# Optimization experiments

Measured on AMD Instinct MI355X. Metric: run time of the kernel, lower is better.

## Reference

```python
import jax, jax.numpy as jnp
import numpy as np
import math

B, S, D = 1, 4096, 512
H, KVH, DH = 8, 4, 64
DH2 = DH // 2
M = int(math.isqrt(S))           # product-key grid side, S == M*M
K = 8                            # top_k
ROPE_BASE = 10000.0


def rope_cos_sin(seq_len, dh, base):
    inv_freq = 1.0 / (base ** (jnp.arange(0, dh, 2, dtype=jnp.float32) / dh))
    t = jnp.arange(seq_len, dtype=jnp.float32)
    freqs = jnp.outer(t, inv_freq)                      # (S, dh/2)
    emb = jnp.concatenate([freqs, freqs], axis=-1)      # (S, dh)
    return jnp.cos(emb), jnp.sin(emb)


def apply_rope(x, cos, sin):
    # x: (B, H, S, dh); half-split rotation (llama-style)
    dh2 = x.shape[-1] // 2
    rot = jnp.concatenate([-x[..., dh2:], x[..., :dh2]], axis=-1)
    return x * cos + rot * sin


def setup_inputs() -> dict:
    key = jax.random.key(0)
    ks = jax.random.split(key, 5)
    s = 0.02
    x = jax.random.normal(ks[0], (B, S, D), dtype=jnp.float32)
    Wq = jax.random.normal(ks[1], (H * DH, D), dtype=jnp.float32) * s
    Wk = jax.random.normal(ks[2], (KVH * DH, D), dtype=jnp.float32) * s
    Wv = jax.random.normal(ks[3], (KVH * DH, D), dtype=jnp.float32) * s
    Wo = jax.random.normal(ks[4], (D, H * DH), dtype=jnp.float32) * s
    return {"x": x, "Wq": Wq, "Wk": Wk, "Wv": Wv, "Wo": Wo}


def reference(x, Wq, Wk, Wv, Wo):
    b, s, d = x.shape
    cos, sin = rope_cos_sin(s, DH, ROPE_BASE)
    q = (x @ Wq.T).reshape(b, s, H, DH).transpose(0, 2, 1, 3)      # (B,H,S,DH)
    k = (x @ Wk.T).reshape(b, s, KVH, DH).transpose(0, 2, 1, 3)    # (B,KVH,S,DH)
    v = (x @ Wv.T).reshape(b, s, KVH, DH).transpose(0, 2, 1, 3)
    q = apply_rope(q, cos, sin)
    k = apply_rope(k, cos, sin)
    rep = H // KVH                                                 # GQA repeat_kv
    k = jnp.repeat(k, rep, axis=1)                                 # (B,H,S,DH)
    v = jnp.repeat(v, rep, axis=1)

    # factorized product keys: sum over grid rows / cols
    kg = k.reshape(b, H, M, M, DH)
    k1 = kg[..., :DH2].sum(axis=-2)                                # (B,H,M,DH2)
    k2 = kg[..., DH2:].sum(axis=-3)                                # (B,H,M,DH2)
    q1, q2 = q[..., :DH2], q[..., DH2:]

    def topk_sel(qh, kh):  # qh: (S,DH2), kh: (M,DH2)
        scores = qh @ kh.T                                         # (S,M)
        _, idx = jax.lax.top_k(scores, K)                          # (S,K)
        return kh[idx], idx                                        # (S,K,DH2), (S,K)

    sel2 = jax.vmap(jax.vmap(topk_sel))
    k1v, i1 = sel2(q1, k1)                                         # (B,H,S,K,DH2)
    k2v, i2 = sel2(q2, k2)

    # cross-product candidates: (B,H,S,K,K,DH) -> (B,H,S,K*K,DH)
    c1 = jnp.broadcast_to(k1v[:, :, :, :, None, :], (b, H, s, K, K, DH2))
    c2 = jnp.broadcast_to(k2v[:, :, :, None, :, :], (b, H, s, K, K, DH2))
    cand = jnp.concatenate([c1, c2], axis=-1).reshape(b, H, s, K * K, DH)

    scores_final = jnp.einsum('bhsd,bhscd->bhsc', q, cand)         # (B,H,S,K*K)
    _, sel = jax.lax.top_k(scores_final, K)                        # (B,H,S,K)
    final_k = jnp.take_along_axis(cand, sel[..., None], axis=3)    # (B,H,S,K,DH)

    row = jnp.take_along_axis(i1, sel // K, axis=3)
    col = jnp.take_along_axis(i2, sel % K, axis=3)
    v_idx = row * M + col                                          # (B,H,S,K)
    final_v = jax.vmap(jax.vmap(lambda vb, ib: vb[ib]))(v, v_idx)  # (B,H,S,K,DH)

    attn = jax.nn.softmax(
        jnp.einsum('bhsd,bhskd->bhsk', q, final_k) / math.sqrt(DH), axis=-1)
    o = jnp.einsum('bhsk,bhskd->bhsd', attn, final_v)              # (B,H,S,DH)
    o = o.transpose(0, 2, 1, 3).reshape(b, s, H * DH)
    return o @ Wo.T
```

## Files before the change

### kernel.cpp

```cpp
#include <hip/hip_runtime.h>
#include <math.h>


static constexpr size_t OFF_P1   = 0;
static constexpr size_t OFF_P2   = 4194304;
static constexpr size_t OFF_KB   = 8388608;
static constexpr size_t OFF_V    = 9437184;
static constexpr size_t OFF_COS  = 10485760;
static constexpr size_t OFF_SIN  = 10616832;
static constexpr size_t OFF_K1   = 10747904;
static constexpr size_t OFF_K2   = 10756096;
static constexpr size_t OFF_O    = 10764288;
static constexpr size_t OFF_PACK = 12861440;

#define LDB 132
#define TILE_F (16 * LDB)

__device__ __forceinline__ float rdlane_f(float v, int lane) {
  return __int_as_float(__builtin_amdgcn_readlane(__float_as_int(v), lane));
}

__global__ __launch_bounds__(256) void freq_table_kernel(float* __restrict__ cosT,
    float* __restrict__ sinT) {
  int idx = blockIdx.x * 256 + threadIdx.x;
  int s = idx >> 5;
  int dp = idx & 31;
  double e = (double)dp * (1.0 / 32.0);
  float pf = (float)pow(10000.0, e);
  float invf = 1.0f / pf;
  float argf = __fmul_rn((float)s, invf);
  cosT[idx] = (float)cos((double)argf);
  sinT[idx] = (float)sin((double)argf);
}

__global__ __launch_bounds__(512) void gemm128_qkv(const float* __restrict__ A,
    const float* __restrict__ Wq, const float* __restrict__ Wk,
    const float* __restrict__ Wv, float* __restrict__ C1,
    float* __restrict__ C2) {
  __shared__ float As[2 * TILE_F];
  __shared__ float Bs[2 * TILE_F];
  const int tid = threadIdx.x;
  const int z = blockIdx.z;
  const int k0 = z ? 384 : 0;
  const int k1 = z ? 512 : 384;
  float* __restrict__ C = z ? C2 : C1;
  const int bm = blockIdx.y, bn = blockIdx.x;
  const int lrow = tid >> 2;
  const int lko = (tid & 3) << 2;
  const int ty = tid >> 4;
  const int tx = tid & 15;
  const float* Bbase = (bn < 4) ? (Wq + ((size_t)bn * 128) * 512)
                     : (bn < 6) ? (Wk + ((size_t)(bn - 4) * 128) * 512)
                                : (Wv + ((size_t)(bn - 6) * 128) * 512);
  const float* Ap = A + (size_t)(bm * 128 + lrow) * 512 + lko;
  const float* Bp = Bbase + (size_t)lrow * 512 + lko;
  float acc[4][8] = {{0.f}};
  float4 a0 = *(const float4*)(Ap + k0);
  float4 b0 = *(const float4*)(Bp + k0);
  int p = 0;
  for (int kt = k0; kt < k1; kt += 16) {
    float* Asp = As + p * TILE_F;
    float* Bsp = Bs + p * TILE_F;
    Asp[(lko + 0) * LDB + lrow] = a0.x;
    Asp[(lko + 1) * LDB + lrow] = a0.y;
    Asp[(lko + 2) * LDB + lrow] = a0.z;
    Asp[(lko + 3) * LDB + lrow] = a0.w;
    Bsp[(lko + 0) * LDB + lrow] = b0.x;
    Bsp[(lko + 1) * LDB + lrow] = b0.y;
    Bsp[(lko + 2) * LDB + lrow] = b0.z;
    Bsp[(lko + 3) * LDB + lrow] = b0.w;
    __syncthreads();
    if (kt + 16 < k1) {
      a0 = *(const float4*)(Ap + kt + 16);
      b0 = *(const float4*)(Bp + kt + 16);
    }
    #pragma unroll
    for (int k = 0; k < 16; ++k) {
      float4 av = *(const float4*)(&Asp[k * LDB + (ty << 2)]);
      float4 bl = *(const float4*)(&Bsp[k * LDB + (tx << 2)]);
      float4 bh = *(const float4*)(&Bsp[k * LDB + 64 + (tx << 2)]);
      float af[4] = {av.x, av.y, av.z, av.w};
      float bf[8] = {bl.x, bl.y, bl.z, bl.w, bh.x, bh.y, bh.z, bh.w};
      #pragma unroll
      for (int i2 = 0; i2 < 4; ++i2)
        #pragma unroll
        for (int j2 = 0; j2 < 8; ++j2)
          acc[i2][j2] = fmaf(af[i2], bf[j2], acc[i2][j2]);
    }
    p ^= 1;
  }
  #pragma unroll
  for (int i2 = 0; i2 < 4; ++i2) {
    int row = bm * 128 + (ty << 2) + i2;
    float* Cp = C + (size_t)row * 1024 + bn * 128;
    *(float4*)(Cp + (tx << 2))      = make_float4(acc[i2][0], acc[i2][1], acc[i2][2], acc[i2][3]);
    *(float4*)(Cp + 64 + (tx << 2)) = make_float4(acc[i2][4], acc[i2][5], acc[i2][6], acc[i2][7]);
  }
}

__global__ __launch_bounds__(512) void gemm128_out(const float* __restrict__ A,
    const float* __restrict__ B, float* __restrict__ Cbase, int N) {
  __shared__ float As[2 * TILE_F];
  __shared__ float Bs[2 * TILE_F];
  const int tid = threadIdx.x;
  const int z = blockIdx.z;
  const int k0 = z << 7;
  const int k1 = k0 + 128;
  float* __restrict__ C = Cbase + (size_t)z * ((size_t)4096 * N);
  const int bm = blockIdx.y, bn = blockIdx.x;
  const int lrow = tid >> 2;
  const int lko = (tid & 3) << 2;
  const int ty = tid >> 4;
  const int tx = tid & 15;
  const float* Ap = A + (size_t)(bm * 128 + lrow) * 512 + lko;
  const float* Bp = B + (size_t)(bn * 128 + lrow) * 512 + lko;
  float acc[4][8] = {{0.f}};
  float4 a0 = *(const float4*)(Ap + k0);
  float4 b0 = *(const float4*)(Bp + k0);
  int p = 0;
  for (int kt = k0; kt < k1; kt += 16) {
    float* Asp = As + p * TILE_F;
    float* Bsp = Bs + p * TILE_F;
    Asp[(lko + 0) * LDB + lrow] = a0.x;
    Asp[(lko + 1) * LDB + lrow] = a0.y;
    Asp[(lko + 2) * LDB + lrow] = a0.z;
    Asp[(lko + 3) * LDB + lrow] = a0.w;
    Bsp[(lko + 0) * LDB + lrow] = b0.x;
    Bsp[(lko + 1) * LDB + lrow] = b0.y;
    Bsp[(lko + 2) * LDB + lrow] = b0.z;
    Bsp[(lko + 3) * LDB + lrow] = b0.w;
    __syncthreads();
    if (kt + 16 < k1) {
      a0 = *(const float4*)(Ap + kt + 16);
      b0 = *(const float4*)(Bp + kt + 16);
    }
    #pragma unroll
    for (int k = 0; k < 16; ++k) {
      float4 av = *(const float4*)(&Asp[k * LDB + (ty << 2)]);
      float4 bl = *(const float4*)(&Bsp[k * LDB + (tx << 2)]);
      float4 bh = *(const float4*)(&Bsp[k * LDB + 64 + (tx << 2)]);
      float af[4] = {av.x, av.y, av.z, av.w};
      float bf[8] = {bl.x, bl.y, bl.z, bl.w, bh.x, bh.y, bh.z, bh.w};
      #pragma unroll
      for (int i2 = 0; i2 < 4; ++i2)
        #pragma unroll
        for (int j2 = 0; j2 < 8; ++j2)
          acc[i2][j2] = fmaf(af[i2], bf[j2], acc[i2][j2]);
    }
    p ^= 1;
  }
  #pragma unroll
  for (int i2 = 0; i2 < 4; ++i2) {
    int row = bm * 128 + (ty << 2) + i2;
    float* Cp = C + (size_t)row * N + bn * 128;
    *(float4*)(Cp + (tx << 2))      = make_float4(acc[i2][0], acc[i2][1], acc[i2][2], acc[i2][3]);
    *(float4*)(Cp + 64 + (tx << 2)) = make_float4(acc[i2][4], acc[i2][5], acc[i2][6], acc[i2][7]);
  }
}

__global__ __launch_bounds__(256) void combine4_kernel(const float* __restrict__ o0,
    const float* __restrict__ o1, const float* __restrict__ o2,
    const float* __restrict__ o3, float* __restrict__ out) {
  int i = blockIdx.x * 256 + threadIdx.x;
  out[i] = __fadd_rn(__fadd_rn(__fadd_rn(o0[i], o1[i]), o2[i]), o3[i]);
}

__global__ __launch_bounds__(256) void kv_rope_kernel(const float* __restrict__ p1,
    const float* __restrict__ p2, const float* __restrict__ cosT,
    const float* __restrict__ sinT, float* __restrict__ kb,
    float* __restrict__ vb) {
  int id = blockIdx.x * 256 + threadIdx.x;
  int s = id >> 9;
  int n = 512 + (id & 511);
  int idx = (s << 10) + n;
  float val = __fadd_rn(p1[idx], p2[idx]);
  int d = n & 63;
  if (n < 768) {
    int pidx = idx ^ 32;
    float pv = __fadd_rn(p1[pidx], p2[pidx]);
    float cs = cosT[(s << 5) + (d & 31)];
    float sn = sinT[(s << 5) + (d & 31)];
    float rot = (d < 32) ? -pv : pv;
    float out = __fadd_rn(__fmul_rn(val, cs), __fmul_rn(rot, sn));
    int kvh = (n - 512) >> 6;
    kb[((size_t)(kvh * 4096 + s) << 6) + d] = out;
  } else {
    int kvh = (n - 768) >> 6;
    vb[((size_t)(kvh * 4096 + s) << 6) + d] = val;
  }
}

__global__ __launch_bounds__(256) void k12_np_kernel(const float* __restrict__ kb,
    float* __restrict__ k1t, float* __restrict__ k2t) {
  int id = blockIdx.x * 256 + threadIdx.x;
  int which = id >> 13;
  int rem = id & 8191;
  int kvh = rem >> 11;
  int rem2 = rem & 2047;
  int i = rem2 >> 5;
  int d = rem2 & 31;
  const float* base = kb + ((size_t)(kvh * 4096) << 6);
  if (which == 0) {
    float acc = base[((size_t)(i * 64) << 6) + d];
    for (int c = 1; c < 64; ++c)
      acc = __fadd_rn(acc, base[((size_t)(i * 64 + c) << 6) + d]);
    k1t[(kvh * 64 + i) * 32 + d] = acc;
  } else {
    float acc = base[((size_t)i << 6) + d + 32];
    for (int r = 1; r < 64; ++r)
      acc = __fadd_rn(acc, base[((size_t)(r * 64 + i) << 6) + d + 32]);
    k2t[(kvh * 64 + i) * 32 + d] = acc;
  }
}

__global__ __launch_bounds__(256) void stage1_sel_kernel(
    const float* __restrict__ p1, const float* __restrict__ p2,
    const float* __restrict__ cosT, const float* __restrict__ sinT,
    const float* __restrict__ k1t, const float* __restrict__ k2t,
    unsigned long long* __restrict__ packs) {
  __shared__ float smem[8704];
  float* qs = smem;
  float* kd = smem + 4352;
  const int t = threadIdx.x;
  const int h = blockIdx.y;
  const int s0 = blockIdx.x * 64;
  const int kvh = h >> 1;
  #pragma unroll
  for (int i = 0; i < 16; ++i) {
    int j = t + i * 256;
    int ss = j >> 6, d = j & 63;
    int s = s0 + ss;
    int idx = (s << 10) + (h << 6) + d;
    float val = __fadd_rn(p1[idx], p2[idx]);
    float pv  = __fadd_rn(p1[idx ^ 32], p2[idx ^ 32]);
    float cs = cosT[(s << 5) + (d & 31)];
    float sn = sinT[(s << 5) + (d & 31)];
    float rot = (d < 32) ? -pv : pv;
    qs[d * 68 + ss] = __fadd_rn(__fmul_rn(val, cs), __fmul_rn(rot, sn));
  }
  #pragma unroll
  for (int i = 0; i < 8; ++i) {
    int j = t + i * 256;
    int r = j >> 5, d = j & 31;
    kd[d * 132 + r]      = k1t[(kvh * 64 + r) * 32 + d];
    kd[d * 132 + 64 + r] = k2t[(kvh * 64 + r) * 32 + d];
  }
  __syncthreads();
  const int ty = t >> 4;
  const int tx = t & 15;
  float acc1[4][4] = {{0.f}};
  float acc2[4][4] = {{0.f}};
  #pragma unroll
  for (int dp = 0; dp < 32; ++dp) {
    float4 kv1 = *(const float4*)&kd[dp * 132 + (ty << 2)];
    float4 kv2 = *(const float4*)&kd[dp * 132 + 64 + (ty << 2)];
    float4 q1 = *(const float4*)&qs[dp * 68 + (tx << 2)];
    float4 q2 = *(const float4*)&qs[(32 + dp) * 68 + (tx << 2)];
    float k1f[4] = {kv1.x, kv1.y, kv1.z, kv1.w};
    float k2f[4] = {kv2.x, kv2.y, kv2.z, kv2.w};
    float q1f[4] = {q1.x, q1.y, q1.z, q1.w};
    float q2f[4] = {q2.x, q2.y, q2.z, q2.w};
    #pragma unroll
    for (int i2 = 0; i2 < 4; ++i2)
      #pragma unroll
      for (int j2 = 0; j2 < 4; ++j2) {
        acc1[i2][j2] = fmaf(k1f[i2], q1f[j2], acc1[i2][j2]);
        acc2[i2][j2] = fmaf(k2f[i2], q2f[j2], acc2[i2][j2]);
      }
  }
  __syncthreads();
  float* sct = smem;
  #pragma unroll
  for (int i2 = 0; i2 < 4; ++i2) {
    int r = (ty << 2) + i2;
    *(float4*)&sct[(size_t)r * 68 + (tx << 2)] =
        make_float4(acc1[i2][0], acc1[i2][1], acc1[i2][2], acc1[i2][3]);
    *(float4*)&sct[(size_t)(64 + r) * 68 + (tx << 2)] =
        make_float4(acc2[i2][0], acc2[i2][1], acc2[i2][2], acc2[i2][3]);
  }
  __syncthreads();
  if (t < 128) {
    int set = t >> 6;
    int sq = t & 63;
    const float* p = sct + (size_t)(set << 6) * 68 + sq;
    float top[8];
    int idx[8];
    #pragma unroll
    for (int u = 0; u < 8; ++u) { top[u] = -INFINITY; idx[u] = 0; }
    #pragma unroll
    for (int r = 0; r < 64; ++r) {
      float v = p[(size_t)r * 68];
      int i = r;
      #pragma unroll
      for (int j = 0; j < 8; ++j) {
        bool gt = v > top[j];
        float tv = top[j]; int ti = idx[j];
        top[j] = gt ? v : tv;
        idx[j] = gt ? i : ti;
        v = gt ? tv : v;
        i = gt ? ti : i;
      }
    }
    unsigned long long pp = 0;
    #pragma unroll
    for (int u = 0; u < 8; ++u) pp |= (unsigned long long)idx[u] << (6 * u);
    packs[(((size_t)(h * 4096 + s0 + sq)) << 1) + set] = pp;
  }
}

__device__ __forceinline__ void bitonic64_val_desc(float& v, int lane) {
  #pragma unroll
  for (int k = 2; k <= 64; k <<= 1) {
    #pragma unroll
    for (int j = k >> 1; j >= 1; j >>= 1) {
      float ov = __shfl_xor(v, j, 64);
      bool up = ((lane & k) == 0) == ((lane & j) == 0);
      float mx = fmaxf(v, ov), mn = fminf(v, ov);
      v = up ? mx : mn;
    }
  }
}

__global__ __launch_bounds__(256) void attn_sel2_kernel(
    const ulonglong2* __restrict__ packs, const float* __restrict__ p1,
    const float* __restrict__ p2, const float* __restrict__ cosT,
    const float* __restrict__ sinT, const float* __restrict__ vb,
    const float* __restrict__ k1t, const float* __restrict__ k2t,
    float* __restrict__ ob) {
  const int lane = threadIdx.x & 63;
  const int w = blockIdx.x * 4 + (threadIdx.x >> 6);
  const int h = w >> 12;
  const int s = w & 4095;
  const int kvh = h >> 1;
  ulonglong2 pk = packs[w];
  const unsigned long long pack1 = pk.x, pack2 = pk.y;
  int qidx = (s << 10) + (h << 6) + lane;
  float vraw = __fadd_rn(p1[qidx], p2[qidx]);
  float pv = __shfl_xor(vraw, 32, 64);
  float cs = cosT[(s << 5) + (lane & 31)];
  float sn = sinT[(s << 5) + (lane & 31)];
  float rot = (lane < 32) ? -pv : pv;
  const float qv = __fadd_rn(__fmul_rn(vraw, cs), __fmul_rn(rot, sn));

  int r1 = (int)((pack1 >> (6 * (lane >> 3))) & 63);
  int r2 = (int)((pack2 >> (6 * (lane & 7))) & 63);
  const float* k1p = k1t + (size_t)(kvh * 64 + r1) * 32;
  const float* k2p = k2t + (size_t)(kvh * 64 + r2) * 32;
  float c = 0.f;
  #pragma unroll
  for (int dq = 0; dq < 32; dq += 4) {
    float4 kk = *(const float4*)(k1p + dq);
    c = __fadd_rn(c, __fmul_rn(rdlane_f(qv, dq + 0), kk.x));
    c = __fadd_rn(c, __fmul_rn(rdlane_f(qv, dq + 1), kk.y));
    c = __fadd_rn(c, __fmul_rn(rdlane_f(qv, dq + 2), kk.z));
    c = __fadd_rn(c, __fmul_rn(rdlane_f(qv, dq + 3), kk.w));
  }
  #pragma unroll
  for (int dq = 0; dq < 32; dq += 4) {
    float4 kk = *(const float4*)(k2p + dq);
    c = __fadd_rn(c, __fmul_rn(rdlane_f(qv, 32 + dq + 0), kk.x));
    c = __fadd_rn(c, __fmul_rn(rdlane_f(qv, 32 + dq + 1), kk.y));
    c = __fadd_rn(c, __fmul_rn(rdlane_f(qv, 32 + dq + 2), kk.z));
    c = __fadd_rn(c, __fmul_rn(rdlane_f(qv, 32 + dq + 3), kk.w));
  }
  const float scand = c;
  float v3 = c;
  bitonic64_val_desc(v3, lane);
  float cvs[8]; int ccs[8];
  unsigned long long used = 0;
  #pragma unroll
  for (int t = 0; t < 8; ++t) {
    float tv = rdlane_f(v3, t);
    unsigned long long m = __ballot(scand == tv) & ~used;
    int ix = __ffsll((long long)m) - 1;
    used |= 1ull << ix;
    cvs[t] = tv;
    ccs[t] = ix;
  }
  float y[8];
  #pragma unroll
  for (int t = 0; t < 8; ++t) y[t] = cvs[t] * 0.125f;
  float mx = y[0];
  #pragma unroll
  for (int t = 1; t < 8; ++t) if (y[t] > mx) mx = y[t];
  float e[8];
  #pragma unroll
  for (int t = 0; t < 8; ++t) e[t] = __expf(__fsub_rn(y[t], mx));
  float wsum = __fadd_rn(__fadd_rn(__fadd_rn(e[0], e[1]), __fadd_rn(e[2], e[3])),
                         __fadd_rn(__fadd_rn(e[4], e[5]), __fadd_rn(e[6], e[7])));
  const float* vbh = vb + ((size_t)kvh << 18);
  float o = 0.f;
  #pragma unroll
  for (int t = 0; t < 8; ++t) {
    float att = __fdiv_rn(e[t], wsum);
    int row = (int)((pack1 >> (6 * (ccs[t] >> 3))) & 63);
    int col = (int)((pack2 >> (6 * (ccs[t] & 7))) & 63);
    o = __fadd_rn(o, __fmul_rn(att, vbh[((size_t)(row * 64 + col) << 6) + lane]));
  }
  ob[(size_t)s * 512 + (h << 6) + lane] = o;
}

extern "C" void kernel_launch(void* const* d_in, const int* in_sizes, int n_in,
                              void* d_out, int out_size, void* d_ws, size_t ws_size,
                              hipStream_t stream) {
  const float* x  = (const float*)d_in[0];
  const float* Wq = (const float*)d_in[1];
  const float* Wk = (const float*)d_in[2];
  const float* Wv = (const float*)d_in[3];
  const float* Wo = (const float*)d_in[4];
  float* ws = (float*)d_ws;
  float* p1   = ws + OFF_P1;
  float* p2   = ws + OFF_P2;
  float* kb   = ws + OFF_KB;
  float* vb   = ws + OFF_V;
  float* cosT = ws + OFF_COS;
  float* sinT = ws + OFF_SIN;
  float* k1t  = ws + OFF_K1;
  float* k2t  = ws + OFF_K2;
  float* ob   = ws + OFF_O;
  unsigned long long* packs = (unsigned long long*)(ws + OFF_PACK);
  float* op = ws + OFF_P1;

  freq_table_kernel<<<512, 256, 0, stream>>>(cosT, sinT);
  gemm128_qkv<<<dim3(8, 32, 2), 512, 0, stream>>>(x, Wq, Wk, Wv, p1, p2);
  kv_rope_kernel<<<8192, 256, 0, stream>>>(p1, p2, cosT, sinT, kb, vb);
  k12_np_kernel<<<64, 256, 0, stream>>>(kb, k1t, k2t);
  stage1_sel_kernel<<<dim3(64, 8), 256, 0, stream>>>(p1, p2, cosT, sinT, k1t, k2t, packs);
  attn_sel2_kernel<<<8192, 256, 0, stream>>>((const ulonglong2*)packs, p1, p2,
                                             cosT, sinT, vb, k1t, k2t, ob);
  gemm128_out<<<dim3(4, 32, 4), 512, 0, stream>>>(ob, Wo, op, 512);
  combine4_kernel<<<8192, 256, 0, stream>>>(op, op + 2097152, op + 4194304,
                                            op + 6291456, (float*)d_out);
}
```

Before: 242.4 us.

## Restructure projection GEMMs to stage only weights in LDS and stream activations

Both the QKV and output projection GEMMs are rewritten so that only a 16x256 weight tile goes through shared memory. Each wave now reads its 8 activation rows directly from global memory as wave-uniform float4 loads, prefetched one k-step ahead. Tiles change from 128x128 to 64x256 and the grid is resized to match. This halves LDS footprint and removes the A-tile stores and barriers. In exchange, activations are re-read from global or cache by every wave, and there is less per-thread register reuse (8x4 outputs per thread).

```diff
diff --git a/kernel.cpp b/kernel.cpp
--- a/kernel.cpp
+++ b/kernel.cpp
@@ -13,8 +13,10 @@
 static constexpr size_t OFF_O    = 10764288;
 static constexpr size_t OFF_PACK = 12861440;
 
-#define LDB 132
-#define TILE_F (16 * LDB)
+#define LDW 256
+#define WTILE (16 * LDW)
+
+#define COMP(v, j) ((j) == 0 ? (v).x : (j) == 1 ? (v).y : (j) == 2 ? (v).z : (v).w)
 
 __device__ __forceinline__ float rdlane_f(float v, int lane) {
   return __int_as_float(__builtin_amdgcn_readlane(__float_as_int(v), lane));
@@ -33,128 +35,155 @@
   sinT[idx] = (float)sin((double)argf);
 }
 
-__global__ __launch_bounds__(512) void gemm128_qkv(const float* __restrict__ A,
+__global__ __launch_bounds__(512, 4) void gemm_qkv_sA(const float* __restrict__ A,
     const float* __restrict__ Wq, const float* __restrict__ Wk,
     const float* __restrict__ Wv, float* __restrict__ C1,
     float* __restrict__ C2) {
-  __shared__ float As[2 * TILE_F];
-  __shared__ float Bs[2 * TILE_F];
+  __shared__ float Ws[2 * WTILE];
   const int tid = threadIdx.x;
   const int z = blockIdx.z;
   const int k0 = z ? 384 : 0;
-  const int k1 = z ? 512 : 384;
+  const int kend = z ? 512 : 384;
   float* __restrict__ C = z ? C2 : C1;
-  const int bm = blockIdx.y, bn = blockIdx.x;
-  const int lrow = tid >> 2;
-  const int lko = (tid & 3) << 2;
-  const int ty = tid >> 4;
-  const int tx = tid & 15;
-  const float* Bbase = (bn < 4) ? (Wq + ((size_t)bn * 128) * 512)
-                     : (bn < 6) ? (Wk + ((size_t)(bn - 4) * 128) * 512)
-                                : (Wv + ((size_t)(bn - 6) * 128) * 512);
-  const float* Ap = A + (size_t)(bm * 128 + lrow) * 512 + lko;
-  const float* Bp = Bbase + (size_t)lrow * 512 + lko;
-  float acc[4][8] = {{0.f}};
-  float4 a0 = *(const float4*)(Ap + k0);
-  float4 b0 = *(const float4*)(Bp + k0);
+  const int bn = blockIdx.x;
+  const int bm = blockIdx.y;
+  const int sn = tid & 255;
+  const int sk = (tid >> 8) << 3;
+  const float* Wbase = (bn < 2) ? (Wq + ((size_t)(bn * 256)) * 512)
+                     : (bn == 2) ? Wk : Wv;
+  const float* Wp = Wbase + (size_t)sn * 512 + sk;
+  const int wid = __builtin_amdgcn_readfirstlane(tid >> 6);
+  const float* Ab = A + (size_t)(bm * 64 + wid * 8) * 512;
+  const int lane = tid & 63;
+  float acc[8][4] = {{0.f}};
+  float4 g0 = *(const float4*)(Wp + k0);
+  float4 g1 = *(const float4*)(Wp + k0 + 4);
   int p = 0;
-  for (int kt = k0; kt < k1; kt += 16) {
-    float* Asp = As + p * TILE_F;
-    float* Bsp = Bs + p * TILE_F;
-    Asp[(lko + 0) * LDB + lrow] = a0.x;
-    Asp[(lko + 1) * LDB + lrow] = a0.y;
-    Asp[(lko + 2) * LDB + lrow] = a0.z;
-    Asp[(lko + 3) * LDB + lrow] = a0.w;
-    Bsp[(lko + 0) * LDB + lrow] = b0.x;
-    Bsp[(lko + 1) * LDB + lrow] = b0.y;
-    Bsp[(lko + 2) * LDB + lrow] = b0.z;
-    Bsp[(lko + 3) * LDB + lrow] = b0.w;
+  for (int kt = k0; kt < kend; kt += 16) {
+    float* Wsp = Ws + p * WTILE;
+    Wsp[(sk + 0) * LDW + sn] = g0.x;
+    Wsp[(sk + 1) * LDW + sn] = g0.y;
+    Wsp[(sk + 2) * LDW + sn] = g0.z;
+    Wsp[(sk + 3) * LDW + sn] = g0.w;
+    Wsp[(sk + 4) * LDW + sn] = g1.x;
+    Wsp[(sk + 5) * LDW + sn] = g1.y;
+    Wsp[(sk + 6) * LDW + sn] = g1.z;
+    Wsp[(sk + 7) * LDW + sn] = g1.w;
     __syncthreads();
-    if (kt + 16 < k1) {
-      a0 = *(const float4*)(Ap + kt + 16);
-      b0 = *(const float4*)(Bp + kt + 16);
-    }
-    #pragma unroll
-    for (int k = 0; k < 16; ++k) {
-      float4 av = *(const float4*)(&Asp[k * LDB + (ty << 2)]);
-      float4 bl = *(const float4*)(&Bsp[k * LDB + (tx << 2)]);
-      float4 bh = *(const float4*)(&Bsp[k * LDB + 64 + (tx << 2)]);
-      float af[4] = {av.x, av.y, av.z, av.w};
-      float bf[8] = {bl.x, bl.y, bl.z, bl.w, bh.x, bh.y, bh.z, bh.w};
+    if (kt + 16 < kend) {
+      g0 = *(const float4*)(Wp + kt + 16);
+      g1 = *(const float4*)(Wp + kt + 20);
+    }
+    float4 a_cur[8];
+    #pragma unroll
+    for (int r = 0; r < 8; ++r)
+      a_cur[r] = *(const float4*)(Ab + (size_t)r * 512 + kt);
+    #pragma unroll
+    for (int k4 = 0; k4 < 16; k4 += 4) {
+      float4 a_nxt[8];
+      if (k4 < 12) {
+        #pragma unroll
+        for (int r = 0; r < 8; ++r)
+          a_nxt[r] = *(const float4*)(Ab + (size_t)r * 512 + kt + k4 + 4);
+      }
       #pragma unroll
-      for (int i2 = 0; i2 < 4; ++i2)
-        #pragma unroll
-        for (int j2 = 0; j2 < 8; ++j2)
-          acc[i2][j2] = fmaf(af[i2], bf[j2], acc[i2][j2]);
+      for (int kk = 0; kk < 4; ++kk) {
+        float4 wv4 = *(const float4*)(&Wsp[(k4 + kk) * LDW + (lane << 2)]);
+        float wf[4] = {wv4.x, wv4.y, wv4.z, wv4.w};
+        #pragma unroll
+        for (int r = 0; r < 8; ++r) {
+          float af = COMP(a_cur[r], kk);
+          #pragma unroll
+          for (int c = 0; c < 4; ++c)
+            acc[r][c] = fmaf(af, wf[c], acc[r][c]);
+        }
+      }
+      if (k4 < 12) {
+        #pragma unroll
+        for (int r = 0; r < 8; ++r) a_cur[r] = a_nxt[r];
+      }
     }
     p ^= 1;
   }
   #pragma unroll
-  for (int i2 = 0; i2 < 4; ++i2) {
-    int row = bm * 128 + (ty << 2) + i2;
-    float* Cp = C + (size_t)row * 1024 + bn * 128;
-    *(float4*)(Cp + (tx << 2))      = make_float4(acc[i2][0], acc[i2][1], acc[i2][2], acc[i2][3]);
-    *(float4*)(Cp + 64 + (tx << 2)) = make_float4(acc[i2][4], acc[i2][5], acc[i2][6], acc[i2][7]);
-  }
-}
-
-__global__ __launch_bounds__(512) void gemm128_out(const float* __restrict__ A,
-    const float* __restrict__ B, float* __restrict__ Cbase, int N) {
-  __shared__ float As[2 * TILE_F];
-  __shared__ float Bs[2 * TILE_F];
+  for (int r = 0; r < 8; ++r) {
+    int row = bm * 64 + wid * 8 + r;
+    float* Cp = C + (size_t)row * 1024 + bn * 256 + (lane << 2);
+    *(float4*)Cp = make_float4(acc[r][0], acc[r][1], acc[r][2], acc[r][3]);
+  }
+}
+
+__global__ __launch_bounds__(512, 4) void gemm_out_sA(const float* __restrict__ A,
+    const float* __restrict__ B, float* __restrict__ Cbase) {
+  __shared__ float Ws[2 * WTILE];
   const int tid = threadIdx.x;
   const int z = blockIdx.z;
   const int k0 = z << 7;
-  const int k1 = k0 + 128;
-  float* __restrict__ C = Cbase + (size_t)z * ((size_t)4096 * N);
-  const int bm = blockIdx.y, bn = blockIdx.x;
-  const int lrow = tid >> 2;
-  const int lko = (tid & 3) << 2;
-  const int ty = tid >> 4;
-  const int tx = tid & 15;
-  const float* Ap = A + (size_t)(bm * 128 + lrow) * 512 + lko;
-  const float* Bp = B + (size_t)(bn * 128 + lrow) * 512 + lko;
-  float acc[4][8] = {{0.f}};
-  float4 a0 = *(const float4*)(Ap + k0);
-  float4 b0 = *(const float4*)(Bp + k0);
+  const int kend = k0 + 128;
+  float* __restrict__ C = Cbase + (size_t)z * ((size_t)4096 * 512);
+  const int bn = blockIdx.x;
+  const int bm = blockIdx.y;
+  const int sn = tid & 255;
+  const int sk = (tid >> 8) << 3;
+  const float* Wp = B + (size_t)(bn * 256 + sn) * 512 + sk;
+  const int wid = __builtin_amdgcn_readfirstlane(tid >> 6);
+  const float* Ab = A + (size_t)(bm * 64 + wid * 8) * 512;
+  const int lane = tid & 63;
+  float acc[8][4] = {{0.f}};
+  float4 g0 = *(const float4*)(Wp + k0);
+  float4 g1 = *(const float4*)(Wp + k0 + 4);
   int p = 0;
-  for (int kt = k0; kt < k1; kt += 16) {
-    float* Asp = As + p * TILE_F;
-    float* Bsp = Bs + p * TILE_F;
-    Asp[(lko + 0) * LDB + lrow] = a0.x;
-    Asp[(lko + 1) * LDB + lrow] = a0.y;
-    Asp[(lko + 2) * LDB + lrow] = a0.z;
-    Asp[(lko + 3) * LDB + lrow] = a0.w;
-    Bsp[(lko + 0) * LDB + lrow] = b0.x;
-    Bsp[(lko + 1) * LDB + lrow] = b0.y;
-    Bsp[(lko + 2) * LDB + lrow] = b0.z;
-    Bsp[(lko + 3) * LDB + lrow] = b0.w;
+  for (int kt = k0; kt < kend; kt += 16) {
+    float* Wsp = Ws + p * WTILE;
+    Wsp[(sk + 0) * LDW + sn] = g0.x;
+    Wsp[(sk + 1) * LDW + sn] = g0.y;
+    Wsp[(sk + 2) * LDW + sn] = g0.z;
+    Wsp[(sk + 3) * LDW + sn] = g0.w;
+    Wsp[(sk + 4) * LDW + sn] = g1.x;
+    Wsp[(sk + 5) * LDW + sn] = g1.y;
+    Wsp[(sk + 6) * LDW + sn] = g1.z;
+    Wsp[(sk + 7) * LDW + sn] = g1.w;
     __syncthreads();
-    if (kt + 16 < k1) {
-      a0 = *(const float4*)(Ap + kt + 16);
-      b0 = *(const float4*)(Bp + kt + 16);
-    }
-    #pragma unroll
-    for (int k = 0; k < 16; ++k) {
-      float4 av = *(const float4*)(&Asp[k * LDB + (ty << 2)]);
-      float4 bl = *(const float4*)(&Bsp[k * LDB + (tx << 2)]);
-      float4 bh = *(const float4*)(&Bsp[k * LDB + 64 + (tx << 2)]);
-      float af[4] = {av.x, av.y, av.z, av.w};
-      float bf[8] = {bl.x, bl.y, bl.z, bl.w, bh.x, bh.y, bh.z, bh.w};
+    if (kt + 16 < kend) {
+      g0 = *(const float4*)(Wp + kt + 16);
+      g1 = *(const float4*)(Wp + kt + 20);
+    }
+    float4 a_cur[8];
+    #pragma unroll
+    for (int r = 0; r < 8; ++r)
+      a_cur[r] = *(const float4*)(Ab + (size_t)r * 512 + kt);
+    #pragma unroll
+    for (int k4 = 0; k4 < 16; k4 += 4) {
+      float4 a_nxt[8];
+      if (k4 < 12) {
+        #pragma unroll
+        for (int r = 0; r < 8; ++r)
+          a_nxt[r] = *(const float4*)(Ab + (size_t)r * 512 + kt + k4 + 4);
+      }
       #pragma unroll
-      for (int i2 = 0; i2 < 4; ++i2)
-        #pragma unroll
-        for (int j2 = 0; j2 < 8; ++j2)
-          acc[i2][j2] = fmaf(af[i2], bf[j2], acc[i2][j2]);
+      for (int kk = 0; kk < 4; ++kk) {
+        float4 wv4 = *(const float4*)(&Wsp[(k4 + kk) * LDW + (lane << 2)]);
+        float wf[4] = {wv4.x, wv4.y, wv4.z, wv4.w};
+        #pragma unroll
+        for (int r = 0; r < 8; ++r) {
+          float af = COMP(a_cur[r], kk);
+          #pragma unroll
+          for (int c = 0; c < 4; ++c)
+            acc[r][c] = fmaf(af, wf[c], acc[r][c]);
+        }
+      }
+      if (k4 < 12) {
+        #pragma unroll
+        for (int r = 0; r < 8; ++r) a_cur[r] = a_nxt[r];
+      }
     }
     p ^= 1;
   }
   #pragma unroll
-  for (int i2 = 0; i2 < 4; ++i2) {
-    int row = bm * 128 + (ty << 2) + i2;
-    float* Cp = C + (size_t)row * N + bn * 128;
-    *(float4*)(Cp + (tx << 2))      = make_float4(acc[i2][0], acc[i2][1], acc[i2][2], acc[i2][3]);
-    *(float4*)(Cp + 64 + (tx << 2)) = make_float4(acc[i2][4], acc[i2][5], acc[i2][6], acc[i2][7]);
+  for (int r = 0; r < 8; ++r) {
+    int row = bm * 64 + wid * 8 + r;
+    float* Cp = C + (size_t)row * 512 + bn * 256 + (lane << 2);
+    *(float4*)Cp = make_float4(acc[r][0], acc[r][1], acc[r][2], acc[r][3]);
   }
 }
 
@@ -422,13 +451,13 @@
   float* op = ws + OFF_P1;
 
   freq_table_kernel<<<512, 256, 0, stream>>>(cosT, sinT);
-  gemm128_qkv<<<dim3(8, 32, 2), 512, 0, stream>>>(x, Wq, Wk, Wv, p1, p2);
+  gemm_qkv_sA<<<dim3(4, 64, 2), 512, 0, stream>>>(x, Wq, Wk, Wv, p1, p2);
   kv_rope_kernel<<<8192, 256, 0, stream>>>(p1, p2, cosT, sinT, kb, vb);
   k12_np_kernel<<<64, 256, 0, stream>>>(kb, k1t, k2t);
   stage1_sel_kernel<<<dim3(64, 8), 256, 0, stream>>>(p1, p2, cosT, sinT, k1t, k2t, packs);
   attn_sel2_kernel<<<8192, 256, 0, stream>>>((const ulonglong2*)packs, p1, p2,
                                              cosT, sinT, vb, k1t, k2t, ob);
-  gemm128_out<<<dim3(4, 32, 4), 512, 0, stream>>>(ob, Wo, op, 512);
+  gemm_out_sA<<<dim3(2, 64, 4), 512, 0, stream>>>(ob, Wo, op);
   combine4_kernel<<<8192, 256, 0, stream>>>(op, op + 2097152, op + 4194304,
                                             op + 6291456, (float*)d_out);
 }
```

New measurement: 288.6 us. 19.1% more time.

## Retile QKV and output GEMMs to 128x64 blocks; fuse K-split into one pass

Applied to the files above, without the earlier changes.

Both fp32 GEMMs move from 128x128 tiles with 512 threads to 128x64 tiles with 256 threads, each thread computing an 8x4 micro-tile. The QKV GEMM drops its z-split over K. A single block now runs the whole K loop, writes the first 384-column partial to C1 partway through, then resets its accumulators and writes the rest to C2. The aim is more blocks for better CU occupancy and less shared-memory use per block. In exchange, each A tile is loaded twice as often across the grid, and the QKV grid has no z dimension, so its blocks run a longer serial K loop.

```diff
diff --git a/kernel.cpp b/kernel.cpp
--- a/kernel.cpp
+++ b/kernel.cpp
@@ -13,8 +13,10 @@
 static constexpr size_t OFF_O    = 10764288;
 static constexpr size_t OFF_PACK = 12861440;
 
-#define LDB 132
-#define TILE_F (16 * LDB)
+#define ALD 132
+#define BLD 68
+#define ATILE (16 * ALD)
+#define BTILE (16 * BLD)
 
 __device__ __forceinline__ float rdlane_f(float v, int lane) {
   return __int_as_float(__builtin_amdgcn_readlane(__float_as_int(v), lane));
@@ -33,128 +35,149 @@
   sinT[idx] = (float)sin((double)argf);
 }
 
-__global__ __launch_bounds__(512) void gemm128_qkv(const float* __restrict__ A,
+__global__ __launch_bounds__(256) void gemm_qkv2(const float* __restrict__ A,
     const float* __restrict__ Wq, const float* __restrict__ Wk,
     const float* __restrict__ Wv, float* __restrict__ C1,
     float* __restrict__ C2) {
-  __shared__ float As[2 * TILE_F];
-  __shared__ float Bs[2 * TILE_F];
+  __shared__ float As[2 * ATILE];
+  __shared__ float Bs[2 * BTILE];
   const int tid = threadIdx.x;
-  const int z = blockIdx.z;
-  const int k0 = z ? 384 : 0;
-  const int k1 = z ? 512 : 384;
-  float* __restrict__ C = z ? C2 : C1;
-  const int bm = blockIdx.y, bn = blockIdx.x;
-  const int lrow = tid >> 2;
-  const int lko = (tid & 3) << 2;
+  const int bn = blockIdx.x;
+  const int bm = blockIdx.y;
+  const float* Bbase = (bn < 8)  ? (Wq + ((size_t)bn * 64) * 512)
+                     : (bn < 12) ? (Wk + ((size_t)(bn - 8) * 64) * 512)
+                                 : (Wv + ((size_t)(bn - 12) * 64) * 512);
+  const int arow = tid >> 1;
+  const int ako  = (tid & 1) << 3;
+  const int brow = tid >> 2;
+  const int bko  = (tid & 3) << 2;
+  const float* Ap = A + (size_t)(bm * 128 + arow) * 512 + ako;
+  const float* Bp = Bbase + (size_t)brow * 512 + bko;
   const int ty = tid >> 4;
   const int tx = tid & 15;
-  const float* Bbase = (bn < 4) ? (Wq + ((size_t)bn * 128) * 512)
-                     : (bn < 6) ? (Wk + ((size_t)(bn - 4) * 128) * 512)
-                                : (Wv + ((size_t)(bn - 6) * 128) * 512);
-  const float* Ap = A + (size_t)(bm * 128 + lrow) * 512 + lko;
-  const float* Bp = Bbase + (size_t)lrow * 512 + lko;
-  float acc[4][8] = {{0.f}};
-  float4 a0 = *(const float4*)(Ap + k0);
-  float4 b0 = *(const float4*)(Bp + k0);
+  float acc[8][4] = {{0.f}};
+  float4 a0 = *(const float4*)(Ap);
+  float4 a1 = *(const float4*)(Ap + 4);
+  float4 b0 = *(const float4*)(Bp);
   int p = 0;
-  for (int kt = k0; kt < k1; kt += 16) {
-    float* Asp = As + p * TILE_F;
-    float* Bsp = Bs + p * TILE_F;
-    Asp[(lko + 0) * LDB + lrow] = a0.x;
-    Asp[(lko + 1) * LDB + lrow] = a0.y;
-    Asp[(lko + 2) * LDB + lrow] = a0.z;
-    Asp[(lko + 3) * LDB + lrow] = a0.w;
-    Bsp[(lko + 0) * LDB + lrow] = b0.x;
-    Bsp[(lko + 1) * LDB + lrow] = b0.y;
-    Bsp[(lko + 2) * LDB + lrow] = b0.z;
-    Bsp[(lko + 3) * LDB + lrow] = b0.w;
+  for (int kt = 0; kt < 512; kt += 16) {
+    float* Asp = As + p * ATILE;
+    float* Bsp = Bs + p * BTILE;
+    Asp[(ako + 0) * ALD + arow] = a0.x;
+    Asp[(ako + 1) * ALD + arow] = a0.y;
+    Asp[(ako + 2) * ALD + arow] = a0.z;
+    Asp[(ako + 3) * ALD + arow] = a0.w;
+    Asp[(ako + 4) * ALD + arow] = a1.x;
+    Asp[(ako + 5) * ALD + arow] = a1.y;
+    Asp[(ako + 6) * ALD + arow] = a1.z;
+    Asp[(ako + 7) * ALD + arow] = a1.w;
+    Bsp[(bko + 0) * BLD + brow] = b0.x;
+    Bsp[(bko + 1) * BLD + brow] = b0.y;
+    Bsp[(bko + 2) * BLD + brow] = b0.z;
+    Bsp[(bko + 3) * BLD + brow] = b0.w;
     __syncthreads();
-    if (kt + 16 < k1) {
+    if (kt + 16 < 512) {
       a0 = *(const float4*)(Ap + kt + 16);
+      a1 = *(const float4*)(Ap + kt + 20);
       b0 = *(const float4*)(Bp + kt + 16);
     }
     #pragma unroll
     for (int k = 0; k < 16; ++k) {
-      float4 av = *(const float4*)(&Asp[k * LDB + (ty << 2)]);
-      float4 bl = *(const float4*)(&Bsp[k * LDB + (tx << 2)]);
-      float4 bh = *(const float4*)(&Bsp[k * LDB + 64 + (tx << 2)]);
-      float af[4] = {av.x, av.y, av.z, av.w};
-      float bf[8] = {bl.x, bl.y, bl.z, bl.w, bh.x, bh.y, bh.z, bh.w};
+      float4 al = *(const float4*)(&Asp[k * ALD + (ty << 3)]);
+      float4 ah = *(const float4*)(&Asp[k * ALD + (ty << 3) + 4]);
+      float4 bv = *(const float4*)(&Bsp[k * BLD + (tx << 2)]);
+      float af[8] = {al.x, al.y, al.z, al.w, ah.x, ah.y, ah.z, ah.w};
+      float bf[4] = {bv.x, bv.y, bv.z, bv.w};
       #pragma unroll
-      for (int i2 = 0; i2 < 4; ++i2)
+      for (int i2 = 0; i2 < 8; ++i2)
         #pragma unroll
-        for (int j2 = 0; j2 < 8; ++j2)
+        for (int j2 = 0; j2 < 4; ++j2)
           acc[i2][j2] = fmaf(af[i2], bf[j2], acc[i2][j2]);
     }
     p ^= 1;
-  }
-  #pragma unroll
-  for (int i2 = 0; i2 < 4; ++i2) {
-    int row = bm * 128 + (ty << 2) + i2;
-    float* Cp = C + (size_t)row * 1024 + bn * 128;
-    *(float4*)(Cp + (tx << 2))      = make_float4(acc[i2][0], acc[i2][1], acc[i2][2], acc[i2][3]);
-    *(float4*)(Cp + 64 + (tx << 2)) = make_float4(acc[i2][4], acc[i2][5], acc[i2][6], acc[i2][7]);
-  }
-}
-
-__global__ __launch_bounds__(512) void gemm128_out(const float* __restrict__ A,
-    const float* __restrict__ B, float* __restrict__ Cbase, int N) {
-  __shared__ float As[2 * TILE_F];
-  __shared__ float Bs[2 * TILE_F];
+    if (kt + 16 == 384) {
+      #pragma unroll
+      for (int i2 = 0; i2 < 8; ++i2) {
+        int row = bm * 128 + (ty << 3) + i2;
+        float* Cp = C1 + (size_t)row * 1024 + bn * 64 + (tx << 2);
+        *(float4*)Cp = make_float4(acc[i2][0], acc[i2][1], acc[i2][2], acc[i2][3]);
+        acc[i2][0] = 0.f; acc[i2][1] = 0.f; acc[i2][2] = 0.f; acc[i2][3] = 0.f;
+      }
+    }
+  }
+  #pragma unroll
+  for (int i2 = 0; i2 < 8; ++i2) {
+    int row = bm * 128 + (ty << 3) + i2;
+    float* Cp = C2 + (size_t)row * 1024 + bn * 64 + (tx << 2);
+    *(float4*)Cp = make_float4(acc[i2][0], acc[i2][1], acc[i2][2], acc[i2][3]);
+  }
+}
+
+__global__ __launch_bounds__(256) void gemm_out2(const float* __restrict__ A,
+    const float* __restrict__ B, float* __restrict__ Cbase) {
+  __shared__ float As[2 * ATILE];
+  __shared__ float Bs[2 * BTILE];
   const int tid = threadIdx.x;
   const int z = blockIdx.z;
   const int k0 = z << 7;
-  const int k1 = k0 + 128;
-  float* __restrict__ C = Cbase + (size_t)z * ((size_t)4096 * N);
-  const int bm = blockIdx.y, bn = blockIdx.x;
-  const int lrow = tid >> 2;
-  const int lko = (tid & 3) << 2;
+  const int kend = k0 + 128;
+  float* __restrict__ C = Cbase + (size_t)z * ((size_t)4096 * 512);
+  const int bn = blockIdx.x;
+  const int bm = blockIdx.y;
+  const int arow = tid >> 1;
+  const int ako  = (tid & 1) << 3;
+  const int brow = tid >> 2;
+  const int bko  = (tid & 3) << 2;
+  const float* Ap = A + (size_t)(bm * 128 + arow) * 512 + ako;
+  const float* Bp = B + (size_t)(bn * 64 + brow) * 512 + bko;
   const int ty = tid >> 4;
   const int tx = tid & 15;
-  const float* Ap = A + (size_t)(bm * 128 + lrow) * 512 + lko;
-  const float* Bp = B + (size_t)(bn * 128 + lrow) * 512 + lko;
-  float acc[4][8] = {{0.f}};
+  float acc[8][4] = {{0.f}};
   float4 a0 = *(const float4*)(Ap + k0);
+  float4 a1 = *(const float4*)(Ap + k0 + 4);
   float4 b0 = *(const float4*)(Bp + k0);
   int p = 0;
-  for (int kt = k0; kt < k1; kt += 16) {
-    float* Asp = As + p * TILE_F;
-    float* Bsp = Bs + p * TILE_F;
-    Asp[(lko + 0) * LDB + lrow] = a0.x;
-    Asp[(lko + 1) * LDB + lrow] = a0.y;
-    Asp[(lko + 2) * LDB + lrow] = a0.z;
-    Asp[(lko + 3) * LDB + lrow] = a0.w;
-    Bsp[(lko + 0) * LDB + lrow] = b0.x;
-    Bsp[(lko + 1) * LDB + lrow] = b0.y;
-    Bsp[(lko + 2) * LDB + lrow] = b0.z;
-    Bsp[(lko + 3) * LDB + lrow] = b0.w;
+  for (int kt = k0; kt < kend; kt += 16) {
+    float* Asp = As + p * ATILE;
+    float* Bsp = Bs + p * BTILE;
+    Asp[(ako + 0) * ALD + arow] = a0.x;
+    Asp[(ako + 1) * ALD + arow] = a0.y;
+    Asp[(ako + 2) * ALD + arow] = a0.z;
+    Asp[(ako + 3) * ALD + arow] = a0.w;
+    Asp[(ako + 4) * ALD + arow] = a1.x;
+    Asp[(ako + 5) * ALD + arow] = a1.y;
+    Asp[(ako + 6) * ALD + arow] = a1.z;
+    Asp[(ako + 7) * ALD + arow] = a1.w;
+    Bsp[(bko + 0) * BLD + brow] = b0.x;
+    Bsp[(bko + 1) * BLD + brow] = b0.y;
+    Bsp[(bko + 2) * BLD + brow] = b0.z;
+    Bsp[(bko + 3) * BLD + brow] = b0.w;
     __syncthreads();
-    if (kt + 16 < k1) {
+    if (kt + 16 < kend) {
       a0 = *(const float4*)(Ap + kt + 16);
+      a1 = *(const float4*)(Ap + kt + 20);
       b0 = *(const float4*)(Bp + kt + 16);
     }
     #pragma unroll
     for (int k = 0; k < 16; ++k) {
-      float4 av = *(const float4*)(&Asp[k * LDB + (ty << 2)]);
-      float4 bl = *(const float4*)(&Bsp[k * LDB + (tx << 2)]);
-      float4 bh = *(const float4*)(&Bsp[k * LDB + 64 + (tx << 2)]);
-      float af[4] = {av.x, av.y, av.z, av.w};
-      float bf[8] = {bl.x, bl.y, bl.z, bl.w, bh.x, bh.y, bh.z, bh.w};
+      float4 al = *(const float4*)(&Asp[k * ALD + (ty << 3)]);
+      float4 ah = *(const float4*)(&Asp[k * ALD + (ty << 3) + 4]);
+      float4 bv = *(const float4*)(&Bsp[k * BLD + (tx << 2)]);
+      float af[8] = {al.x, al.y, al.z, al.w, ah.x, ah.y, ah.z, ah.w};
+      float bf[4] = {bv.x, bv.y, bv.z, bv.w};
       #pragma unroll
-      for (int i2 = 0; i2 < 4; ++i2)
+      for (int i2 = 0; i2 < 8; ++i2)
         #pragma unroll
-        for (int j2 = 0; j2 < 8; ++j2)
+        for (int j2 = 0; j2 < 4; ++j2)
           acc[i2][j2] = fmaf(af[i2], bf[j2], acc[i2][j2]);
     }
     p ^= 1;
   }
   #pragma unroll
-  for (int i2 = 0; i2 < 4; ++i2) {
-    int row = bm * 128 + (ty << 2) + i2;
-    float* Cp = C + (size_t)row * N + bn * 128;
-    *(float4*)(Cp + (tx << 2))      = make_float4(acc[i2][0], acc[i2][1], acc[i2][2], acc[i2][3]);
-    *(float4*)(Cp + 64 + (tx << 2)) = make_float4(acc[i2][4], acc[i2][5], acc[i2][6], acc[i2][7]);
+  for (int i2 = 0; i2 < 8; ++i2) {
+    int row = bm * 128 + (ty << 3) + i2;
+    float* Cp = C + (size_t)row * 512 + bn * 64 + (tx << 2);
+    *(float4*)Cp = make_float4(acc[i2][0], acc[i2][1], acc[i2][2], acc[i2][3]);
   }
 }
 
@@ -422,13 +445,13 @@
   float* op = ws + OFF_P1;
 
   freq_table_kernel<<<512, 256, 0, stream>>>(cosT, sinT);
-  gemm128_qkv<<<dim3(8, 32, 2), 512, 0, stream>>>(x, Wq, Wk, Wv, p1, p2);
+  gemm_qkv2<<<dim3(16, 32), 256, 0, stream>>>(x, Wq, Wk, Wv, p1, p2);
   kv_rope_kernel<<<8192, 256, 0, stream>>>(p1, p2, cosT, sinT, kb, vb);
   k12_np_kernel<<<64, 256, 0, stream>>>(kb, k1t, k2t);
   stage1_sel_kernel<<<dim3(64, 8), 256, 0, stream>>>(p1, p2, cosT, sinT, k1t, k2t, packs);
   attn_sel2_kernel<<<8192, 256, 0, stream>>>((const ulonglong2*)packs, p1, p2,
                                              cosT, sinT, vb, k1t, k2t, ob);
-  gemm128_out<<<dim3(4, 32, 4), 512, 0, stream>>>(ob, Wo, op, 512);
+  gemm_out2<<<dim3(8, 32, 4), 256, 0, stream>>>(ob, Wo, op);
   combine4_kernel<<<8192, 256, 0, stream>>>(op, op + 2097152, op + 4194304,
                                             op + 6291456, (float*)d_out);
 }
```

New measurement: 250.0 us. +3.2%, slower.
